# Kernel optimization log

Hardware: AMD Instinct MI355X
Metric: run time of the kernel (lower is better)

The kernel has to match this reference:

```python
import jax, jax.numpy as jnp
import numpy as np

N = 50000          # nodes
E = 1_600_000      # edges (avg degree 32)
D = 128            # feature dim (in == out)
R = 8              # relation types
LN_EPS = 1e-5


def setup_inputs() -> dict:
    key = jax.random.key(0)
    ks = jax.random.split(key, 6)
    x = jax.random.normal(ks[0], (N, D), dtype=jnp.float32)
    edge_index = jax.random.randint(ks[1], (2, E), 0, N, dtype=jnp.int64)
    edge_type = jax.random.randint(ks[2], (E,), 0, R, dtype=jnp.int64)
    W_rel = jax.random.normal(ks[3], (R, D, D), dtype=jnp.float32) / np.float32(np.sqrt(D))
    W_root = jax.random.normal(ks[4], (D, D), dtype=jnp.float32) / np.float32(np.sqrt(D))
    bias = jnp.zeros((D,), jnp.float32)
    gamma = jnp.ones((D,), jnp.float32)
    beta = jnp.zeros((D,), jnp.float32)
    return dict(x=x, edge_index=edge_index, edge_type=edge_type, node_num=N,
                W_rel=W_rel, W_root=W_root, bias=bias, gamma=gamma, beta=beta)


def reference(x, edge_index, edge_type, node_num, W_rel, W_root, bias, gamma, beta):
    src, dst = edge_index[0], edge_index[1]
    # Relational conv: transform once per relation, then gather per edge.
    xw = jnp.einsum('nd,rdf->rnf', x, W_rel)          # [R, N, D]
    msg = xw[edge_type, src]                           # [E, D]
    # Per-(dst, relation) mean normalization (PyG RGCNConv 'mean' aggr per relation).
    key_idx = dst * R + edge_type                      # [E]
    cnt = jax.ops.segment_sum(jnp.ones((E,), x.dtype), key_idx, num_segments=N * R)
    norm = 1.0 / jnp.maximum(cnt[key_idx], 1.0)        # [E]
    agg = jax.ops.segment_sum(msg * norm[:, None], dst, num_segments=N)  # [N, D]
    feat = agg + x @ W_root + bias                     # self-loop + bias
    feat = feat[:node_num]                             # keep real nodes only
    # norm -> act -> dropout(eval=identity) fusion chain
    mu = jnp.mean(feat, axis=-1, keepdims=True)
    var = jnp.var(feat, axis=-1, keepdims=True)
    feat = (feat - mu) * jax.lax.rsqrt(var + LN_EPS) * gamma + beta
    return jax.nn.relu(feat)
```

## Files before the change

kernel.cpp:

```cpp
#include <hip/hip_runtime.h>
#include <hip/hip_bf16.h>
#include <cstdint>

#define N_NODES 50000
#define N_EDGES 1600000
#define DIM 128
#define NREL 8
#define LN_EPS 1e-5f

#define NKEYS (N_NODES * NREL)
#define SCAN_CHUNK 1024
#define SCAN_NBLK ((NKEYS + SCAN_CHUNK - 1) / SCAN_CHUNK)

#define A_STRIDE 136
#define B_STRIDE 136

#define CNT_BLOCKS ((N_EDGES + 255) / 256)
#define XB_BLOCKS 6250
#define BT_BLOCKS 576

typedef unsigned short ushort_t;
typedef short short8 __attribute__((ext_vector_type(8)));
typedef float f32x4 __attribute__((ext_vector_type(4)));
typedef unsigned uintx4 __attribute__((ext_vector_type(4)));

__device__ inline ushort_t f2bf(float f) {
    union { float f; unsigned u; } v; v.f = f;
    unsigned r = (v.u + 0x7FFFu + ((v.u >> 16) & 1u)) >> 16;
    return (ushort_t)r;
}
__device__ inline float bf_lo(unsigned u) {
    union { unsigned u; float f; } v; v.u = u << 16;
    return v.f;
}
__device__ inline float bf_hi(unsigned u) {
    union { unsigned u; float f; } v; v.u = u & 0xffff0000u;
    return v.f;
}

__global__ __launch_bounds__(256) void prep_kernel(const float* __restrict__ x,
                                                   ushort_t* __restrict__ xb,
                                                   const float* __restrict__ W_rel,
                                                   const float* __restrict__ W_root,
                                                   ushort_t* __restrict__ Bt,
                                                   const int* __restrict__ ei,
                                                   const int* __restrict__ et,
                                                   unsigned* __restrict__ cnt,
                                                   unsigned* __restrict__ krk) {
    int b = blockIdx.x;
    if (b < CNT_BLOCKS) {
        int e = b * 256 + threadIdx.x;
        if (e < N_EDGES) {
            int dst = ei[N_EDGES + e];
            unsigned key = (unsigned)dst * NREL + (unsigned)et[e];
            unsigned rank = atomicAdd(&cnt[key], 1u);
            krk[e] = (key << 13) | rank;
        }
    } else if (b < CNT_BLOCKS + XB_BLOCKS) {
        int i = (b - CNT_BLOCKS) * 256 + threadIdx.x;
        float4 v = ((const float4*)x)[i];
        unsigned lo = (unsigned)f2bf(v.x) | ((unsigned)f2bf(v.y) << 16);
        unsigned hi = (unsigned)f2bf(v.z) | ((unsigned)f2bf(v.w) << 16);
        ((uint2*)xb)[i] = make_uint2(lo, hi);
    } else if (b < CNT_BLOCKS + XB_BLOCKS + BT_BLOCKS) {
        int i = (b - CNT_BLOCKS - XB_BLOCKS) * 256 + threadIdx.x;
        int r   = i >> 14;
        int rem = i & 16383;
        int n   = rem >> 7;
        int k   = rem & 127;
        const float* W = (r < NREL) ? (W_rel + (size_t)r * DIM * DIM) : W_root;
        Bt[i] = f2bf(W[(size_t)k * DIM + n]);
    } else {
        if (threadIdx.x < 32)
            ((uint2*)(xb + (size_t)N_NODES * DIM))[threadIdx.x] = make_uint2(0u, 0u);
    }
}

__global__ __launch_bounds__(256) void scan1_kernel(const unsigned* __restrict__ cnt,
                                                    uint2* __restrict__ meta,
                                                    unsigned* __restrict__ bsums) {
    __shared__ unsigned lds[256];
    int tid = threadIdx.x;
    int i0  = blockIdx.x * SCAN_CHUNK + tid * 4;
    unsigned v[4], incl[4];
    unsigned s = 0;
#pragma unroll
    for (int j = 0; j < 4; ++j) {
        v[j] = (i0 + j < NKEYS) ? cnt[i0 + j] : 0u;
        s += v[j];
        incl[j] = s;
    }
    lds[tid] = s;
    __syncthreads();
    for (int off = 1; off < 256; off <<= 1) {
        unsigned a = (tid >= off) ? lds[tid - off] : 0u;
        __syncthreads();
        lds[tid] += a;
        __syncthreads();
    }
    unsigned base = lds[tid] - s;
#pragma unroll
    for (int j = 0; j < 4; ++j) {
        if (i0 + j < NKEYS) meta[i0 + j] = make_uint2(base + incl[j] - v[j], v[j]);
    }
    if (tid == 255) bsums[blockIdx.x] = lds[255];
}

__global__ __launch_bounds__(512) void scan2_kernel(unsigned* __restrict__ bsums) {
    __shared__ unsigned lds[512];
    int tid = threadIdx.x;
    unsigned v = (tid < SCAN_NBLK) ? bsums[tid] : 0u;
    lds[tid] = v;
    __syncthreads();
    for (int off = 1; off < 512; off <<= 1) {
        unsigned a = (tid >= off) ? lds[tid - off] : 0u;
        __syncthreads();
        lds[tid] += a;
        __syncthreads();
    }
    if (tid < SCAN_NBLK) bsums[tid] = lds[tid] - v;
}

__global__ __launch_bounds__(256) void fill_kernel(const int* __restrict__ ei,
                                                   const unsigned* __restrict__ krk,
                                                   const uint2* __restrict__ meta,
                                                   const unsigned* __restrict__ bsums,
                                                   int* __restrict__ sorted_src) {
    int e = blockIdx.x * 256 + threadIdx.x;
    if (e < N_EDGES) {
        unsigned kr   = krk[e];
        unsigned key  = kr >> 13;
        unsigned rank = kr & 8191u;
        unsigned p = meta[key].x + bsums[key >> 10] + rank;
        sorted_src[p] = ei[e];
    }
}

__global__ __launch_bounds__(256) void aggregate_kernel(const uint2* __restrict__ meta,
                                                        const unsigned* __restrict__ bsums,
                                                        const int* __restrict__ sorted_src,
                                                        const ushort_t* __restrict__ xb,
                                                        ushort_t* __restrict__ h,
                                                        int r0, int cr) {
    int hw = threadIdx.x >> 5;
    int sl = threadIdx.x & 31;
    int g0 = blockIdx.x * 16 + hw * 2;
    int g1 = g0 + 1;
    int total = N_NODES * cr;
    if (g0 >= total) return;

    unsigned st0, mc0, st1 = 0u, mc1 = 0u;
    if (cr == NREL) {
        uint4 mm = *(const uint4*)&meta[(unsigned)g0];
        unsigned bs = bsums[(unsigned)g0 >> 10];
        st0 = mm.x + bs; mc0 = mm.y;
        st1 = mm.z + bs; mc1 = mm.w;
    } else {
        int n0 = g0 / cr, rl0 = g0 - n0 * cr;
        unsigned key0 = (unsigned)n0 * NREL + (unsigned)(r0 + rl0);
        uint2 md0 = meta[key0];
        st0 = md0.x + bsums[key0 >> 10];
        mc0 = md0.y;
        if (g1 < total) {
            int n1 = g1 / cr, rl1 = g1 - n1 * cr;
            unsigned key1 = (unsigned)n1 * NREL + (unsigned)(r0 + rl1);
            uint2 md1 = meta[key1];
            st1 = md1.x + bsums[key1 >> 10];
            mc1 = md1.y;
        }
    }

    float a00 = 0.f, a01 = 0.f, a02 = 0.f, a03 = 0.f;
    float a10 = 0.f, a11 = 0.f, a12 = 0.f, a13 = 0.f;
    const char* xbase = (const char*)xb;
    unsigned slb = (unsigned)sl << 3;

    unsigned c0 = 0, c1 = 0;
    while (c0 < mc0 || c1 < mc1) {
        int sv0 = (c0 + (unsigned)sl < mc0) ? sorted_src[st0 + c0 + sl] : N_NODES;
        int sv1 = (c1 + (unsigned)sl < mc1) ? sorted_src[st1 + c1 + sl] : N_NODES;
        unsigned rem0 = (c0 < mc0) ? ((mc0 - c0 > 32u) ? 32u : (mc0 - c0)) : 0u;
        unsigned rem1 = (c1 < mc1) ? ((mc1 - c1 > 32u) ? 32u : (mc1 - c1)) : 0u;
        unsigned rm = rem0 > rem1 ? rem0 : rem1;
        for (unsigned j = 0; j < rm; j += 4) {
            int s00 = __shfl(sv0, (int)j,     32);
            int s01 = __shfl(sv0, (int)j + 1, 32);
            int s02 = __shfl(sv0, (int)j + 2, 32);
            int s03 = __shfl(sv0, (int)j + 3, 32);
            int s10 = __shfl(sv1, (int)j,     32);
            int s11 = __shfl(sv1, (int)j + 1, 32);
            int s12 = __shfl(sv1, (int)j + 2, 32);
            int s13 = __shfl(sv1, (int)j + 3, 32);
            uint2 d00 = *(const uint2*)(xbase + ((((unsigned)s00) << 8) | slb));
            uint2 d01 = *(const uint2*)(xbase + ((((unsigned)s01) << 8) | slb));
            uint2 d02 = *(const uint2*)(xbase + ((((unsigned)s02) << 8) | slb));
            uint2 d03 = *(const uint2*)(xbase + ((((unsigned)s03) << 8) | slb));
            uint2 d10 = *(const uint2*)(xbase + ((((unsigned)s10) << 8) | slb));
            uint2 d11 = *(const uint2*)(xbase + ((((unsigned)s11) << 8) | slb));
            uint2 d12 = *(const uint2*)(xbase + ((((unsigned)s12) << 8) | slb));
            uint2 d13 = *(const uint2*)(xbase + ((((unsigned)s13) << 8) | slb));
            a00 += (bf_lo(d00.x) + bf_lo(d01.x)) + (bf_lo(d02.x) + bf_lo(d03.x));
            a01 += (bf_hi(d00.x) + bf_hi(d01.x)) + (bf_hi(d02.x) + bf_hi(d03.x));
            a02 += (bf_lo(d00.y) + bf_lo(d01.y)) + (bf_lo(d02.y) + bf_lo(d03.y));
            a03 += (bf_hi(d00.y) + bf_hi(d01.y)) + (bf_hi(d02.y) + bf_hi(d03.y));
            a10 += (bf_lo(d10.x) + bf_lo(d11.x)) + (bf_lo(d12.x) + bf_lo(d13.x));
            a11 += (bf_hi(d10.x) + bf_hi(d11.x)) + (bf_hi(d12.x) + bf_hi(d13.x));
            a12 += (bf_lo(d10.y) + bf_lo(d11.y)) + (bf_lo(d12.y) + bf_lo(d13.y));
            a13 += (bf_hi(d10.y) + bf_hi(d11.y)) + (bf_hi(d12.y) + bf_hi(d13.y));
        }
        c0 += rem0;
        c1 += rem1;
    }

    float inv0 = 1.0f / fmaxf((float)mc0, 1.0f);
    unsigned lo0 = (unsigned)f2bf(a00 * inv0) | ((unsigned)f2bf(a01 * inv0) << 16);
    unsigned hi0 = (unsigned)f2bf(a02 * inv0) | ((unsigned)f2bf(a03 * inv0) << 16);
    ((uint2*)(h + (size_t)g0 * DIM))[sl] = make_uint2(lo0, hi0);
    if (g1 < total) {
        float inv1 = 1.0f / fmaxf((float)mc1, 1.0f);
        unsigned lo1 = (unsigned)f2bf(a10 * inv1) | ((unsigned)f2bf(a11 * inv1) << 16);
        unsigned hi1 = (unsigned)f2bf(a12 * inv1) | ((unsigned)f2bf(a13 * inv1) << 16);
        ((uint2*)(h + (size_t)g1 * DIM))[sl] = make_uint2(lo1, hi1);
    }
}

__global__ __launch_bounds__(512) void gemm_ln_kernel(const ushort_t* __restrict__ h,
                                                      int cr, int r0,
                                                      const ushort_t* __restrict__ xb,
                                                      const ushort_t* __restrict__ Bt,
                                                      int include_root,
                                                      const float* __restrict__ bias,
                                                      const float* __restrict__ gamma,
                                                      const float* __restrict__ beta,
                                                      float* __restrict__ out,
                                                      int accumulate, int do_ln) {
    __shared__ __align__(16) ushort_t As[128 * A_STRIDE];
    __shared__ __align__(16) ushort_t Bs[128 * B_STRIDE];

    int tid  = threadIdx.x;
    int w    = tid >> 6;
    int lane = tid & 63;
    int m    = lane & 15;
    int quad = lane >> 4;
    int n0   = blockIdx.x * 128;

    f32x4 acc[8];
#pragma unroll
    for (int j = 0; j < 8; ++j) acc[j] = (f32x4){0.f, 0.f, 0.f, 0.f};

    int nrel = cr + include_root;
    for (int rr = 0; rr < nrel; ++rr) {
        int rel = (rr < cr) ? (r0 + rr) : NREL;

#pragma unroll
        for (int p = 0; p < 4; ++p) {
            int c = tid + 512 * p;
            int row = c >> 4, ch = c & 15;
            uintx4 v = *(const uintx4*)(Bt + ((size_t)rel * DIM + row) * DIM + ch * 8);
            *(uintx4*)&Bs[row * B_STRIDE + ch * 8] = v;
        }
#pragma unroll
        for (int p = 0; p < 4; ++p) {
            int c = tid + 512 * p;
            int row = c >> 4, ch = c & 15;
            uintx4 v = (uintx4){0u, 0u, 0u, 0u};
            int node = n0 + row;
            if (node < N_NODES) {
                const ushort_t* src = (rr < cr)
                    ? (h + ((size_t)node * cr + rr) * DIM)
                    : (xb + (size_t)node * DIM);
                v = *(const uintx4*)(src + ch * 8);
            }
            *(uintx4*)&As[row * A_STRIDE + ch * 8] = v;
        }
        __syncthreads();

#pragma unroll
        for (int t = 0; t < 4; ++t) {
            short8 af = *(const short8*)&As[(w * 16 + m) * A_STRIDE + t * 32 + quad * 8];
#pragma unroll
            for (int j = 0; j < 8; ++j) {
                short8 bf = *(const short8*)&Bs[(j * 16 + m) * B_STRIDE + t * 32 + quad * 8];
                acc[j] = __builtin_amdgcn_mfma_f32_16x16x32_bf16(af, bf, acc[j], 0, 0, 0);
            }
        }
        __syncthreads();
    }

    if (do_ln) {
        float bj[8], gj[8], btj[8];
#pragma unroll
        for (int j = 0; j < 8; ++j) {
            bj[j]  = bias[j * 16 + m];
            gj[j]  = gamma[j * 16 + m];
            btj[j] = beta[j * 16 + m];
        }
#pragma unroll
        for (int i = 0; i < 4; ++i) {
            float s = 0.f, sq = 0.f;
#pragma unroll
            for (int j = 0; j < 8; ++j) {
                float v = acc[j][i] + bj[j];
                s  += v;
                sq += v * v;
            }
#pragma unroll
            for (int off = 1; off < 16; off <<= 1) {
                s  += __shfl_xor(s, off, 64);
                sq += __shfl_xor(sq, off, 64);
            }
            float mean = s * (1.0f / DIM);
            float var  = sq * (1.0f / DIM) - mean * mean;
            float rstd = rsqrtf(var + LN_EPS);
            int node = n0 + w * 16 + quad * 4 + i;
            if (node < N_NODES) {
#pragma unroll
                for (int j = 0; j < 8; ++j) {
                    float v = acc[j][i] + bj[j];
                    v = (v - mean) * rstd * gj[j] + btj[j];
                    out[(size_t)node * DIM + j * 16 + m] = fmaxf(v, 0.f);
                }
            }
        }
    } else {
#pragma unroll
        for (int i = 0; i < 4; ++i) {
            int node = n0 + w * 16 + quad * 4 + i;
            if (node < N_NODES) {
#pragma unroll
                for (int j = 0; j < 8; ++j) {
                    size_t o = (size_t)node * DIM + j * 16 + m;
                    float v = acc[j][i];
                    if (accumulate) v += out[o];
                    out[o] = v;
                }
            }
        }
    }
}

__global__ __launch_bounds__(256) void ln_kernel(float* __restrict__ out,
                                                 const float* __restrict__ bias,
                                                 const float* __restrict__ gamma,
                                                 const float* __restrict__ beta) {
    int row  = blockIdx.x * 4 + (threadIdx.x >> 6);
    int lane = threadIdx.x & 63;
    if (row >= N_NODES) return;
    float2 v = *(float2*)(out + (size_t)row * DIM + lane * 2);
    float2 bi = *(const float2*)(bias + lane * 2);
    v.x += bi.x;
    v.y += bi.y;
    float s  = v.x + v.y;
    float sq = v.x * v.x + v.y * v.y;
#pragma unroll
    for (int off = 32; off > 0; off >>= 1) {
        s  += __shfl_xor(s, off, 64);
        sq += __shfl_xor(sq, off, 64);
    }
    float mean = s * (1.0f / DIM);
    float var  = sq * (1.0f / DIM) - mean * mean;
    float rstd = rsqrtf(var + LN_EPS);
    float2 g = *(const float2*)(gamma + lane * 2);
    float2 b = *(const float2*)(beta + lane * 2);
    v.x = fmaxf((v.x - mean) * rstd * g.x + b.x, 0.f);
    v.y = fmaxf((v.y - mean) * rstd * g.y + b.y, 0.f);
    *(float2*)(out + (size_t)row * DIM + lane * 2) = v;
}

extern "C" void kernel_launch(void* const* d_in, const int* in_sizes, int n_in,
                              void* d_out, int out_size, void* d_ws, size_t ws_size,
                              hipStream_t stream) {
    const float* x      = (const float*)d_in[0];
    const int*   ei     = (const int*)d_in[1];
    const int*   et     = (const int*)d_in[2];
    const float* W_rel  = (const float*)d_in[4];
    const float* W_root = (const float*)d_in[5];
    const float* bias   = (const float*)d_in[6];
    const float* gamma  = (const float*)d_in[7];
    const float* beta   = (const float*)d_in[8];
    float*       out    = (float*)d_out;

    char* ws = (char*)d_ws;
    size_t off = 0;
    auto alloc = [&](size_t bytes) { char* p = ws + off; off = (off + bytes + 255) & ~(size_t)255; return p; };
    unsigned* cnt        = (unsigned*)alloc((size_t)NKEYS * 4);
    uint2*    meta       = (uint2*)alloc((size_t)NKEYS * 8);
    unsigned* bsums      = (unsigned*)alloc((size_t)SCAN_NBLK * 4);
    unsigned* krk        = (unsigned*)alloc((size_t)N_EDGES * 4);
    int*      sorted_src = (int*)alloc((size_t)N_EDGES * 4);
    ushort_t* Bt         = (ushort_t*)alloc((size_t)9 * DIM * DIM * 2);
    ushort_t* xb         = (ushort_t*)alloc((size_t)(N_NODES + 1) * DIM * 2);
    size_t fixedOff = off;
    ushort_t* h = (ushort_t*)(ws + fixedOff);
    size_t availB = ws_size > fixedOff ? ws_size - fixedOff : 0;
    size_t perRel = (size_t)N_NODES * DIM * 2;
    int chunkR = (int)(availB / perRel);
    if (chunkR > NREL) chunkR = NREL;
    if (chunkR < 1)    chunkR = 1;

    hipMemsetAsync(cnt, 0, (size_t)NKEYS * 4, stream);
    prep_kernel<<<CNT_BLOCKS + XB_BLOCKS + BT_BLOCKS + 1, 256, 0, stream>>>(
        x, xb, W_rel, W_root, Bt, ei, et, cnt, krk);
    scan1_kernel<<<SCAN_NBLK, 256, 0, stream>>>(cnt, meta, bsums);
    scan2_kernel<<<1, 512, 0, stream>>>(bsums);
    fill_kernel<<<(N_EDGES + 255) / 256, 256, 0, stream>>>(ei, krk, meta, bsums, sorted_src);

    int gemmGrid = (N_NODES + 127) / 128;

    if (chunkR >= NREL) {
        int nbuck = N_NODES * NREL;
        aggregate_kernel<<<(nbuck + 15) / 16, 256, 0, stream>>>(meta, bsums, sorted_src,
                                                                xb, h, 0, NREL);
        gemm_ln_kernel<<<gemmGrid, 512, 0, stream>>>(h, NREL, 0, xb, Bt, 1,
                                                     bias, gamma, beta, out, 0, 1);
    } else {
        for (int r0 = 0; r0 < NREL; r0 += chunkR) {
            int cr = (NREL - r0 < chunkR) ? (NREL - r0) : chunkR;
            int nbuck = N_NODES * cr;
            aggregate_kernel<<<(nbuck + 15) / 16, 256, 0, stream>>>(meta, bsums, sorted_src,
                                                                    xb, h, r0, cr);
            int include_root = (r0 + cr == NREL) ? 1 : 0;
            gemm_ln_kernel<<<gemmGrid, 512, 0, stream>>>(h, cr, r0, xb, Bt, include_root,
                                                         bias, gamma, beta, out,
                                                         r0 > 0 ? 1 : 0, 0);
        }
        ln_kernel<<<(N_NODES + 3) / 4, 256, 0, stream>>>(out, bias, gamma, beta);
    }
}
```

Baseline: 314.7 us.

## Replace global-atomic counting sort with two-level LDS-histogram bucket sort

The edge bucketing by (dst, relation) moves from global atomics on 400K counters plus a scattered fill to a two-pass radix-style sort. Per-block shared-memory histograms over coarse bins of 1024 keys are scanned, edges are scattered into bins, then each bin is sorted locally in LDS to produce meta and sorted_src. This is meant to remove contended global atomics, the memset and random scattered writes. In exchange it adds two extra kernels and an extra pass over the edges.

Result: faster. 255.1 us (-19.0%).

```diff
diff --git a/kernel.cpp b/kernel.cpp
--- a/kernel.cpp
+++ b/kernel.cpp
@@ -9,13 +9,13 @@
 #define LN_EPS 1e-5f
 
 #define NKEYS (N_NODES * NREL)
-#define SCAN_CHUNK 1024
-#define SCAN_NBLK ((NKEYS + SCAN_CHUNK - 1) / SCAN_CHUNK)
+#define PA_BLOCKS ((N_EDGES + 1023) / 1024)
+#define NBIN ((NKEYS + 1023) / 1024)
+#define BH_STRIDE 1600
 
 #define A_STRIDE 136
 #define B_STRIDE 136
 
-#define CNT_BLOCKS ((N_EDGES + 255) / 256)
 #define XB_BLOCKS 6250
 #define BT_BLOCKS 576
 
@@ -45,25 +45,34 @@
                                                    ushort_t* __restrict__ Bt,
                                                    const int* __restrict__ ei,
                                                    const int* __restrict__ et,
-                                                   unsigned* __restrict__ cnt,
-                                                   unsigned* __restrict__ krk) {
+                                                   unsigned* __restrict__ block_hist) {
     int b = blockIdx.x;
-    if (b < CNT_BLOCKS) {
-        int e = b * 256 + threadIdx.x;
-        if (e < N_EDGES) {
-            int dst = ei[N_EDGES + e];
-            unsigned key = (unsigned)dst * NREL + (unsigned)et[e];
-            unsigned rank = atomicAdd(&cnt[key], 1u);
-            krk[e] = (key << 13) | rank;
-        }
-    } else if (b < CNT_BLOCKS + XB_BLOCKS) {
-        int i = (b - CNT_BLOCKS) * 256 + threadIdx.x;
+    int tid = threadIdx.x;
+    if (b < PA_BLOCKS) {
+        __shared__ unsigned hist[NBIN];
+        for (int i = tid; i < NBIN; i += 256) hist[i] = 0u;
+        __syncthreads();
+        int e = b * 1024 + tid;
+#pragma unroll
+        for (int q = 0; q < 4; ++q) {
+            int eq = e + q * 256;
+            if (eq < N_EDGES) {
+                int dst = ei[N_EDGES + eq];
+                unsigned key = (unsigned)dst * NREL + (unsigned)et[eq];
+                atomicAdd(&hist[key >> 10], 1u);
+            }
+        }
+        __syncthreads();
+        for (int i = tid; i < NBIN; i += 256)
+            block_hist[(size_t)i * BH_STRIDE + b] = hist[i];
+    } else if (b < PA_BLOCKS + XB_BLOCKS) {
+        int i = (b - PA_BLOCKS) * 256 + tid;
         float4 v = ((const float4*)x)[i];
         unsigned lo = (unsigned)f2bf(v.x) | ((unsigned)f2bf(v.y) << 16);
         unsigned hi = (unsigned)f2bf(v.z) | ((unsigned)f2bf(v.w) << 16);
         ((uint2*)xb)[i] = make_uint2(lo, hi);
-    } else if (b < CNT_BLOCKS + XB_BLOCKS + BT_BLOCKS) {
-        int i = (b - CNT_BLOCKS - XB_BLOCKS) * 256 + threadIdx.x;
+    } else if (b < PA_BLOCKS + XB_BLOCKS + BT_BLOCKS) {
+        int i = (b - PA_BLOCKS - XB_BLOCKS) * 256 + tid;
         int r   = i >> 14;
         int rem = i & 16383;
         int n   = rem >> 7;
@@ -71,22 +80,114 @@
         const float* W = (r < NREL) ? (W_rel + (size_t)r * DIM * DIM) : W_root;
         Bt[i] = f2bf(W[(size_t)k * DIM + n]);
     } else {
-        if (threadIdx.x < 32)
-            ((uint2*)(xb + (size_t)N_NODES * DIM))[threadIdx.x] = make_uint2(0u, 0u);
-    }
-}
-
-__global__ __launch_bounds__(256) void scan1_kernel(const unsigned* __restrict__ cnt,
+        if (tid < 32)
+            ((uint2*)(xb + (size_t)N_NODES * DIM))[tid] = make_uint2(0u, 0u);
+    }
+}
+
+__global__ __launch_bounds__(256) void scanA2_kernel(unsigned* __restrict__ bh,
+                                                     unsigned* __restrict__ bin_tot) {
+    __shared__ unsigned lds[256];
+    int k = blockIdx.x;
+    int tid = threadIdx.x;
+    unsigned* row = bh + (size_t)k * BH_STRIDE;
+    int base = tid * 7;
+    unsigned v[7];
+    unsigned s = 0;
+#pragma unroll
+    for (int j = 0; j < 7; ++j) {
+        int i = base + j;
+        v[j] = (i < PA_BLOCKS) ? row[i] : 0u;
+        s += v[j];
+    }
+    lds[tid] = s;
+    __syncthreads();
+    for (int off = 1; off < 256; off <<= 1) {
+        unsigned a = (tid >= off) ? lds[tid - off] : 0u;
+        __syncthreads();
+        lds[tid] += a;
+        __syncthreads();
+    }
+    unsigned ex = lds[tid] - s;
+#pragma unroll
+    for (int j = 0; j < 7; ++j) {
+        int i = base + j;
+        if (i < PA_BLOCKS) {
+            unsigned t = v[j];
+            row[i] = ex;
+            ex += t;
+        }
+    }
+    if (tid == 255) bin_tot[k] = lds[255];
+}
+
+__global__ __launch_bounds__(512) void scanA3_kernel(const unsigned* __restrict__ bin_tot,
+                                                     unsigned* __restrict__ bin_base) {
+    __shared__ unsigned lds[512];
+    int tid = threadIdx.x;
+    unsigned v = (tid < NBIN) ? bin_tot[tid] : 0u;
+    lds[tid] = v;
+    __syncthreads();
+    for (int off = 1; off < 512; off <<= 1) {
+        unsigned a = (tid >= off) ? lds[tid - off] : 0u;
+        __syncthreads();
+        lds[tid] += a;
+        __syncthreads();
+    }
+    if (tid < NBIN) bin_base[tid] = lds[tid] - v;
+}
+
+__global__ __launch_bounds__(256) void passB_kernel(const int* __restrict__ ei,
+                                                    const int* __restrict__ et,
+                                                    const unsigned* __restrict__ bh,
+                                                    const unsigned* __restrict__ bin_base,
+                                                    unsigned* __restrict__ rec) {
+    __shared__ unsigned col[NBIN];
+    __shared__ unsigned rk[NBIN];
+    int b = blockIdx.x;
+    int tid = threadIdx.x;
+    for (int i = tid; i < NBIN; i += 256) {
+        col[i] = bin_base[i] + bh[(size_t)i * BH_STRIDE + b];
+        rk[i]  = 0u;
+    }
+    __syncthreads();
+    int e = b * 1024 + tid;
+#pragma unroll
+    for (int q = 0; q < 4; ++q) {
+        int eq = e + q * 256;
+        if (eq < N_EDGES) {
+            int src = ei[eq];
+            int dst = ei[N_EDGES + eq];
+            unsigned key = (unsigned)dst * NREL + (unsigned)et[eq];
+            unsigned bin = key >> 10;
+            unsigned r = atomicAdd(&rk[bin], 1u);
+            rec[col[bin] + r] = ((unsigned)src << 10) | (key & 1023u);
+        }
+    }
+}
+
+__global__ __launch_bounds__(256) void passC_kernel(const unsigned* __restrict__ rec,
+                                                    const unsigned* __restrict__ bin_base,
+                                                    const unsigned* __restrict__ bin_tot,
                                                     uint2* __restrict__ meta,
-                                                    unsigned* __restrict__ bsums) {
+                                                    int* __restrict__ sorted_src) {
+    __shared__ unsigned cnt[1024];
     __shared__ unsigned lds[256];
+    int k = blockIdx.x;
     int tid = threadIdx.x;
-    int i0  = blockIdx.x * SCAN_CHUNK + tid * 4;
-    unsigned v[4], incl[4];
-    unsigned s = 0;
+    unsigned base = bin_base[k];
+    unsigned tot  = bin_tot[k];
+    for (int i = tid; i < 1024; i += 256) cnt[i] = 0u;
+    __syncthreads();
+    for (unsigned i = tid; i < tot; i += 256) {
+        unsigned r = rec[base + i];
+        atomicAdd(&cnt[r & 1023u], 1u);
+    }
+    __syncthreads();
+    unsigned v[4], incl[4], s = 0;
 #pragma unroll
     for (int j = 0; j < 4; ++j) {
-        v[j] = (i0 + j < NKEYS) ? cnt[i0 + j] : 0u;
+        v[j] = cnt[tid * 4 + j];
         s += v[j];
         incl[j] = s;
     }
@@ -98,46 +199,26 @@
         lds[tid] += a;
         __syncthreads();
     }
-    unsigned base = lds[tid] - s;
+    unsigned bs = lds[tid] - s;
+    unsigned key0 = (unsigned)k * 1024 + tid * 4;
 #pragma unroll
     for (int j = 0; j < 4; ++j) {
-        if (i0 + j < NKEYS) meta[i0 + j] = make_uint2(base + incl[j] - v[j], v[j]);
-    }
-    if (tid == 255) bsums[blockIdx.x] = lds[255];
-}
-
-__global__ __launch_bounds__(512) void scan2_kernel(unsigned* __restrict__ bsums) {
-    __shared__ unsigned lds[512];
-    int tid = threadIdx.x;
-    unsigned v = (tid < SCAN_NBLK) ? bsums[tid] : 0u;
-    lds[tid] = v;
-    __syncthreads();
-    for (int off = 1; off < 512; off <<= 1) {
-        unsigned a = (tid >= off) ? lds[tid - off] : 0u;
-        __syncthreads();
-        lds[tid] += a;
-        __syncthreads();
-    }
-    if (tid < SCAN_NBLK) bsums[tid] = lds[tid] - v;
-}
-
-__global__ __launch_bounds__(256) void fill_kernel(const int* __restrict__ ei,
-                                                   const unsigned* __restrict__ krk,
-                                                   const uint2* __restrict__ meta,
-                                                   const unsigned* __restrict__ bsums,
-                                                   int* __restrict__ sorted_src) {
-    int e = blockIdx.x * 256 + threadIdx.x;
-    if (e < N_EDGES) {
-        unsigned kr   = krk[e];
-        unsigned key  = kr >> 13;
-        unsigned rank = kr & 8191u;
-        unsigned p = meta[key].x + bsums[key >> 10] + rank;
-        sorted_src[p] = ei[e];
+        unsigned ex = bs + incl[j] - v[j];
+        if (key0 + j < NKEYS) meta[key0 + j] = make_uint2(base + ex, v[j]);
+    }
+    __syncthreads();
+#pragma unroll
+    for (int j = 0; j < 4; ++j) cnt[tid * 4 + j] = bs + incl[j] - v[j];
+    __syncthreads();
+    for (unsigned i = tid; i < tot; i += 256) {
+        unsigned r = rec[base + i];
+        unsigned q = r & 1023u;
+        unsigned p = atomicAdd(&cnt[q], 1u);
+        sorted_src[base + p] = (int)(r >> 10);
     }
 }
 
 __global__ __launch_bounds__(256) void aggregate_kernel(const uint2* __restrict__ meta,
-                                                        const unsigned* __restrict__ bsums,
                                                         const int* __restrict__ sorted_src,
                                                         const ushort_t* __restrict__ xb,
                                                         ushort_t* __restrict__ h,
@@ -152,21 +233,18 @@
     unsigned st0, mc0, st1 = 0u, mc1 = 0u;
     if (cr == NREL) {
         uint4 mm = *(const uint4*)&meta[(unsigned)g0];
-        unsigned bs = bsums[(unsigned)g0 >> 10];
-        st0 = mm.x + bs; mc0 = mm.y;
-        st1 = mm.z + bs; mc1 = mm.w;
+        st0 = mm.x; mc0 = mm.y;
+        st1 = mm.z; mc1 = mm.w;
     } else {
         int n0 = g0 / cr, rl0 = g0 - n0 * cr;
         unsigned key0 = (unsigned)n0 * NREL + (unsigned)(r0 + rl0);
         uint2 md0 = meta[key0];
-        st0 = md0.x + bsums[key0 >> 10];
-        mc0 = md0.y;
+        st0 = md0.x; mc0 = md0.y;
         if (g1 < total) {
             int n1 = g1 / cr, rl1 = g1 - n1 * cr;
             unsigned key1 = (unsigned)n1 * NREL + (unsigned)(r0 + rl1);
             uint2 md1 = meta[key1];
-            st1 = md1.x + bsums[key1 >> 10];
-            mc1 = md1.y;
+            st1 = md1.x; mc1 = md1.y;
         }
     }
 
@@ -383,10 +461,11 @@
     char* ws = (char*)d_ws;
     size_t off = 0;
     auto alloc = [&](size_t bytes) { char* p = ws + off; off = (off + bytes + 255) & ~(size_t)255; return p; };
-    unsigned* cnt        = (unsigned*)alloc((size_t)NKEYS * 4);
+    unsigned* block_hist = (unsigned*)alloc((size_t)NBIN * BH_STRIDE * 4);
+    unsigned* bin_tot    = (unsigned*)alloc((size_t)NBIN * 4);
+    unsigned* bin_base   = (unsigned*)alloc((size_t)NBIN * 4);
+    unsigned* rec        = (unsigned*)alloc((size_t)N_EDGES * 4);
     uint2*    meta       = (uint2*)alloc((size_t)NKEYS * 8);
-    unsigned* bsums      = (unsigned*)alloc((size_t)SCAN_NBLK * 4);
-    unsigned* krk        = (unsigned*)alloc((size_t)N_EDGES * 4);
     int*      sorted_src = (int*)alloc((size_t)N_EDGES * 4);
     ushort_t* Bt         = (ushort_t*)alloc((size_t)9 * DIM * DIM * 2);
     ushort_t* xb         = (ushort_t*)alloc((size_t)(N_NODES + 1) * DIM * 2);
@@ -398,18 +477,18 @@
     if (chunkR > NREL) chunkR = NREL;
     if (chunkR < 1)    chunkR = 1;
 
-    hipMemsetAsync(cnt, 0, (size_t)NKEYS * 4, stream);
-    prep_kernel<<<CNT_BLOCKS + XB_BLOCKS + BT_BLOCKS + 1, 256, 0, stream>>>(
-        x, xb, W_rel, W_root, Bt, ei, et, cnt, krk);
-    scan1_kernel<<<SCAN_NBLK, 256, 0, stream>>>(cnt, meta, bsums);
-    scan2_kernel<<<1, 512, 0, stream>>>(bsums);
-    fill_kernel<<<(N_EDGES + 255) / 256, 256, 0, stream>>>(ei, krk, meta, bsums, sorted_src);
+    prep_kernel<<<PA_BLOCKS + XB_BLOCKS + BT_BLOCKS + 1, 256, 0, stream>>>(
+        x, xb, W_rel, W_root, Bt, ei, et, block_hist);
+    scanA2_kernel<<<NBIN, 256, 0, stream>>>(block_hist, bin_tot);
+    scanA3_kernel<<<1, 512, 0, stream>>>(bin_tot, bin_base);
+    passB_kernel<<<PA_BLOCKS, 256, 0, stream>>>(ei, et, block_hist, bin_base, rec);
+    passC_kernel<<<NBIN, 256, 0, stream>>>(rec, bin_base, bin_tot, meta, sorted_src);
 
     int gemmGrid = (N_NODES + 127) / 128;
 
     if (chunkR >= NREL) {
         int nbuck = N_NODES * NREL;
-        aggregate_kernel<<<(nbuck + 15) / 16, 256, 0, stream>>>(meta, bsums, sorted_src,
+        aggregate_kernel<<<(nbuck + 15) / 16, 256, 0, stream>>>(meta, sorted_src,
                                                                 xb, h, 0, NREL);
         gemm_ln_kernel<<<gemmGrid, 512, 0, stream>>>(h, NREL, 0, xb, Bt, 1,
                                                      bias, gamma, beta, out, 0, 1);
@@ -417,7 +496,7 @@
         for (int r0 = 0; r0 < NREL; r0 += chunkR) {
             int cr = (NREL - r0 < chunkR) ? (NREL - r0) : chunkR;
             int nbuck = N_NODES * cr;
-            aggregate_kernel<<<(nbuck + 15) / 16, 256, 0, stream>>>(meta, bsums, sorted_src,
+            aggregate_kernel<<<(nbuck + 15) / 16, 256, 0, stream>>>(meta, sorted_src,
                                                                     xb, h, r0, cr);
             int include_root = (r0 + cr == NREL) ? 1 : 0;
             gemm_ln_kernel<<<gemmGrid, 512, 0, stream>>>(h, cr, r0, xb, Bt, include_root,
```
